# Kernel optimization log

Measured on AMD Instinct MI355X. Metric: run time of the kernel, lower is better.

## Reference

```python
import jax, jax.numpy as jnp
import numpy as np

N = 25000   # nodes
E = 400000  # edges
F_IN = 128  # in_features
F_E = 16    # edge_features
C = 32      # channel_width
F_OUT = 1   # out_features
SLOPE = 0.01  # torch LeakyReLU default negative_slope


def leaky_relu(x):
    return jnp.where(x >= 0, x, SLOPE * x)


def setup_inputs() -> dict:
    key = jax.random.key(0)
    ks = jax.random.split(key, 12)
    x = jax.random.normal(ks[0], (N, F_IN), dtype=jnp.float32)
    edge_index = jax.random.randint(ks[1], (2, E), 0, N, dtype=jnp.int64)
    edge_attr = jax.random.normal(ks[2], (E, F_E), dtype=jnp.float32)
    # parameters (scaled like kaiming-ish fan-in init)
    W_in = jax.random.normal(ks[3], (F_IN, C), dtype=jnp.float32) / np.sqrt(F_IN)
    b_in = jnp.zeros((C,), dtype=jnp.float32)
    W_edge = jax.random.normal(ks[4], (F_E, C * C), dtype=jnp.float32) / np.sqrt(F_E)
    b_edge = jnp.zeros((C * C,), dtype=jnp.float32)
    W_root = jax.random.normal(ks[5], (C, C), dtype=jnp.float32) / np.sqrt(C)
    b_conv = jnp.zeros((C,), dtype=jnp.float32)
    W_out = jax.random.normal(ks[6], (C, F_OUT), dtype=jnp.float32) / np.sqrt(C)
    b_out = jnp.zeros((F_OUT,), dtype=jnp.float32)
    return {
        "x": x, "edge_index": edge_index, "edge_attr": edge_attr,
        "W_in": W_in, "b_in": b_in, "W_edge": W_edge, "b_edge": b_edge,
        "W_root": W_root, "b_conv": b_conv, "W_out": W_out, "b_out": b_out,
    }


def reference(x, edge_index, edge_attr, W_in, b_in, W_edge, b_edge,
              W_root, b_conv, W_out, b_out):
    # input projection (dropout = identity in eval mode)
    h = leaky_relu(x @ W_in + b_in)                       # [N, C]

    # NNConv layer (gnn_depth = 1):
    # per-edge weight matrix from edge_nn: Linear + LeakyReLU
    We = leaky_relu(edge_attr @ W_edge + b_edge)          # [E, C*C]
    We = We.reshape(E, C, C)                              # [E, C, C]
    src, dst = edge_index[0], edge_index[1]               # PyG: j=source, i=target
    # gather source node features, per-edge matvec, scatter-add to targets
    msg = jnp.einsum('ec,eco->eo', h[src], We)            # [E, C]
    aggr = jax.ops.segment_sum(msg, dst, num_segments=N)  # [N, C]
    h = aggr + h @ W_root + b_conv                        # root weight + bias
    h = leaky_relu(h)

    return h @ W_out + b_out                              # [N, F_OUT]
```

## Files before the change

### kernel.cpp

```cpp
#include <hip/hip_runtime.h>

#define NN 25000
#define EE 400000
#define FIN 128
#define FE 16
#define CH 32
#define SLOPE 0.01f

typedef __attribute__((ext_vector_type(8))) short bf16x8;
typedef __attribute__((ext_vector_type(4))) float f32x4;

__device__ __forceinline__ float lrelu(float v) { return fmaxf(v, SLOPE * v); }

__device__ __forceinline__ short f2bf(float f) {
    union { float f; unsigned u; } v; v.f = f;
    unsigned r = (v.u + 0x7fffu + ((v.u >> 16) & 1u)) >> 16;
    return (short)r;
}

__global__ void __launch_bounds__(256)
k_input_proj(const float* __restrict__ x,
             const float* __restrict__ W_in,
             const float* __restrict__ b_in,
             float* __restrict__ h) {
    __shared__ short Wt1[CH * 136];
    int tid = threadIdx.x;
#pragma unroll
    for (int i = 0; i < 16; i++) {
        int id = tid + 256 * i;
        int k = id >> 5, c = id & 31;
        Wt1[c * 136 + k] = f2bf(W_in[id]);
    }
    __syncthreads();

    int wave = tid >> 6, lane = tid & 63;
    int n16 = lane & 15, quad = lane >> 4;
    int node0 = blockIdx.x * 64 + wave * 16;

    f32x4 D[2];
#pragma unroll
    for (int ch = 0; ch < 2; ch++) {
        float bb = b_in[ch * 16 + n16];
        D[ch] = (f32x4){bb, bb, bb, bb};
    }
    int arow = node0 + n16; if (arow >= NN) arow = NN - 1;
#pragma unroll
    for (int kb = 0; kb < 4; kb++) {
        const float4* xp = (const float4*)(x + (size_t)arow * FIN + kb * 32 + quad * 8);
        float4 xa = xp[0], xb = xp[1];
        bf16x8 A = (bf16x8){f2bf(xa.x), f2bf(xa.y), f2bf(xa.z), f2bf(xa.w),
                            f2bf(xb.x), f2bf(xb.y), f2bf(xb.z), f2bf(xb.w)};
#pragma unroll
        for (int ch = 0; ch < 2; ch++) {
            bf16x8 B = *(const bf16x8*)&Wt1[(ch * 16 + n16) * 136 + kb * 32 + quad * 8];
            D[ch] = __builtin_amdgcn_mfma_f32_16x16x32_bf16(A, B, D[ch], 0, 0, 0);
        }
    }
#pragma unroll
    for (int ch = 0; ch < 2; ch++)
#pragma unroll
        for (int r = 0; r < 4; r++) {
            int nn = node0 + quad * 4 + r;
            if (nn < NN) h[(size_t)nn * CH + ch * 16 + n16] = lrelu(D[ch][r]);
        }
}

__global__ void __launch_bounds__(256, 2)
k_edge(const float* __restrict__ ea,
       const float* __restrict__ W_edge,
       const float* __restrict__ b_edge,
       const int* __restrict__ src,
       const int* __restrict__ dst,
       const float* __restrict__ h,
       float* __restrict__ aggr) {
    __shared__ short WtL[1024 * 16];
    __shared__ float bseg[1024];
    __shared__ float hsL[128 * 36];
    __shared__ short zslot[8];

    int tid = threadIdx.x;
    int e0 = blockIdx.x * 128;

    if (tid < 8) zslot[tid] = 0;
#pragma unroll
    for (int i = 0; i < 4; i++) {
        int co = tid + 256 * i;
        short cv[16];
#pragma unroll
        for (int k = 0; k < 16; k++) cv[k] = f2bf(W_edge[k * 1024 + co]);
        ((bf16x8*)&WtL[co * 16])[0] = *(bf16x8*)&cv[0];
        ((bf16x8*)&WtL[co * 16])[1] = *(bf16x8*)&cv[8];
        bseg[co] = b_edge[co];
    }
    {
        int e = tid >> 1, half = tid & 1;
        int s = src[e0 + e];
        const float4* hp = (const float4*)(h + (size_t)s * CH + half * 16);
        float* wdst = &hsL[e * 36 + half * 16];
#pragma unroll
        for (int j = 0; j < 4; j++) *(float4*)(wdst + j * 4) = hp[j];
    }
    __syncthreads();

    int wave = tid >> 6, lane = tid & 63;
    int n16 = lane & 15, quad = lane >> 4;
    int t0 = wave * 32, t1 = wave * 32 + 16;

    bf16x8 A0 = (bf16x8){0,0,0,0,0,0,0,0}, A1 = A0;
    if (quad < 2) {
        const float4* p0 = (const float4*)(ea + (size_t)(e0 + t0 + n16) * FE + quad * 8);
        const float4* p1 = (const float4*)(ea + (size_t)(e0 + t1 + n16) * FE + quad * 8);
        float4 a = p0[0], b = p0[1];
        A0 = (bf16x8){f2bf(a.x), f2bf(a.y), f2bf(a.z), f2bf(a.w),
                      f2bf(b.x), f2bf(b.y), f2bf(b.z), f2bf(b.w)};
        a = p1[0]; b = p1[1];
        A1 = (bf16x8){f2bf(a.x), f2bf(a.y), f2bf(a.z), f2bf(a.w),
                      f2bf(b.x), f2bf(b.y), f2bf(b.z), f2bf(b.w)};
    }

    f32x4 m0[2], m1[2];
    m0[0] = (f32x4){0,0,0,0}; m0[1] = m0[0]; m1[0] = m0[0]; m1[1] = m0[0];

    const short* bbase = (quad < 2) ? WtL : zslot;
    int bstride = (quad < 2) ? 1 : 0;

#pragma unroll 1
    for (int c4 = 0; c4 < 8; c4++) {
        f32x4 hv0[4], hv1[4];
#pragma unroll
        for (int r = 0; r < 4; r++) {
            hv0[r] = *(const f32x4*)&hsL[(t0 + quad * 4 + r) * 36 + c4 * 4];
            hv1[r] = *(const f32x4*)&hsL[(t1 + quad * 4 + r) * 36 + c4 * 4];
        }
#pragma unroll
        for (int cc = 0; cc < 4; cc++) {
            int c = c4 * 4 + cc;
#pragma unroll
            for (int oh = 0; oh < 2; oh++) {
                int cb = c * 2 + oh;
                bf16x8 B = *(const bf16x8*)&bbase[bstride * ((cb * 16 + n16) * 16 + quad * 8)];
                float bb = bseg[cb * 16 + n16];
                f32x4 Cb = (f32x4){bb, bb, bb, bb};
                f32x4 D0 = __builtin_amdgcn_mfma_f32_16x16x32_bf16(A0, B, Cb, 0, 0, 0);
                f32x4 D1 = __builtin_amdgcn_mfma_f32_16x16x32_bf16(A1, B, Cb, 0, 0, 0);
#pragma unroll
                for (int r = 0; r < 4; r++) {
                    m0[oh][r] = fmaf(hv0[r][cc], lrelu(D0[r]), m0[oh][r]);
                    m1[oh][r] = fmaf(hv1[r][cc], lrelu(D1[r]), m1[oh][r]);
                }
            }
        }
    }

#pragma unroll
    for (int r = 0; r < 4; r++) {
        int ed0 = dst[e0 + t0 + quad * 4 + r];
        int ed1 = dst[e0 + t1 + quad * 4 + r];
#pragma unroll
        for (int oh = 0; oh < 2; oh++) {
            unsafeAtomicAdd(&aggr[(size_t)ed0 * CH + oh * 16 + n16], m0[oh][r]);
            unsafeAtomicAdd(&aggr[(size_t)ed1 * CH + oh * 16 + n16], m1[oh][r]);
        }
    }
}

__global__ void k_node(const float* __restrict__ aggr,
                       const float* __restrict__ h,
                       const float* __restrict__ W_root,
                       const float* __restrict__ b_conv,
                       const float* __restrict__ W_out,
                       const float* __restrict__ b_out,
                       float* __restrict__ out) {
    __shared__ float Wr[CH * CH];
    __shared__ float Wo[CH];
    __shared__ float bc[CH];
    int tid = threadIdx.x;
    for (int i = tid; i < CH * CH / 4; i += 256)
        ((float4*)Wr)[i] = ((const float4*)W_root)[i];
    if (tid < CH / 4) ((float4*)Wo)[tid] = ((const float4*)W_out)[tid];
    else if (tid >= 8 && tid < 8 + CH / 4) ((float4*)bc)[tid - 8] = ((const float4*)b_conv)[tid - 8];
    __syncthreads();
    int n = blockIdx.x * 256 + tid;
    if (n >= NN) return;
    float hr[CH], ag[CH];
#pragma unroll
    for (int i = 0; i < CH / 4; i++) {
        ((float4*)hr)[i] = ((const float4*)(h + (size_t)n * CH))[i];
        ((float4*)ag)[i] = ((const float4*)(aggr + (size_t)n * CH))[i];
    }
    float acc = b_out[0];
#pragma unroll 1
    for (int o = 0; o < CH; o++) {
        float t = ag[o] + bc[o];
#pragma unroll
        for (int c = 0; c < CH; c++) t = fmaf(hr[c], Wr[c * CH + o], t);
        acc = fmaf(lrelu(t), Wo[o], acc);
    }
    out[n] = acc;
}

extern "C" void kernel_launch(void* const* d_in, const int* in_sizes, int n_in,
                              void* d_out, int out_size, void* d_ws, size_t ws_size,
                              hipStream_t stream) {
    const float* x      = (const float*)d_in[0];
    const int*   ei     = (const int*)d_in[1];
    const float* ea     = (const float*)d_in[2];
    const float* W_in   = (const float*)d_in[3];
    const float* b_in   = (const float*)d_in[4];
    const float* W_edge = (const float*)d_in[5];
    const float* b_edge = (const float*)d_in[6];
    const float* W_root = (const float*)d_in[7];
    const float* b_conv = (const float*)d_in[8];
    const float* W_out  = (const float*)d_in[9];
    const float* b_out  = (const float*)d_in[10];
    float* out  = (float*)d_out;
    float* h    = (float*)d_ws;
    float* aggr = h + (size_t)NN * CH;

    hipMemsetAsync(aggr, 0, (size_t)NN * CH * sizeof(float), stream);
    k_input_proj<<<(NN + 63) / 64, 256, 0, stream>>>(x, W_in, b_in, h);
    k_edge<<<EE / 128, 256, 0, stream>>>(ea, W_edge, b_edge, ei, ei + EE, h, aggr);
    k_node<<<(NN + 255) / 256, 256, 0, stream>>>(aggr, h, W_root, b_conv, W_out, b_out, out);
}
```

Baseline: 200.8 us.

## Precompute bf16 edge weights and attrs in a fused pre-kernel, raise edge occupancy

The input projection kernel gains auxiliary blocks that transpose W_edge to bf16 once, zero the aggregation buffer in place of a memset, and convert edge_attr to bf16 in global memory. The edge kernel then copies the prepared weight tile with vector loads instead of converting W_edge in every block. It also drops the shared bias array, reading b_edge from global, and raises launch bounds to 3 blocks per CU. The node kernel stores W_root transposed so each output reads contiguous vector rows. The trade-off is an extra bf16 copy of edge_attr written and read back through global memory, plus bias loads moved into the inner loop.

```diff
diff --git a/kernel.cpp b/kernel.cpp
--- a/kernel.cpp
+++ b/kernel.cpp
@@ -6,6 +6,8 @@
 #define FE 16
 #define CH 32
 #define SLOPE 0.01f
+#define PROJ_BLOCKS 391
+#define AUX_BLOCKS 64
 
 typedef __attribute__((ext_vector_type(8))) short bf16x8;
 typedef __attribute__((ext_vector_type(4))) float f32x4;
@@ -19,12 +21,32 @@
 }
 
 __global__ void __launch_bounds__(256)
-k_input_proj(const float* __restrict__ x,
-             const float* __restrict__ W_in,
-             const float* __restrict__ b_in,
-             float* __restrict__ h) {
+k_pre(const float* __restrict__ x, const float* __restrict__ W_in,
+      const float* __restrict__ b_in, const float* __restrict__ ea,
+      const float* __restrict__ W_edge,
+      float* __restrict__ h, float* __restrict__ aggr,
+      short* __restrict__ WtT, short* __restrict__ ea_bf) {
     __shared__ short Wt1[CH * 136];
     int tid = threadIdx.x;
+
+    if (blockIdx.x >= PROJ_BLOCKS) {
+        int t = (blockIdx.x - PROJ_BLOCKS) * 256 + tid;
+        { int co = t >> 4, k = t & 15; WtT[t] = f2bf(W_edge[k * 1024 + co]); }
+        float4 z = make_float4(0.f, 0.f, 0.f, 0.f);
+        for (int i = t; i < NN * CH / 4; i += AUX_BLOCKS * 256) ((float4*)aggr)[i] = z;
+        for (int e = t; e < EE; e += AUX_BLOCKS * 256) {
+            const float4* p = (const float4*)(ea + (size_t)e * FE);
+            float4 a0 = p[0], a1 = p[1], a2 = p[2], a3 = p[3];
+            bf16x8 lo = (bf16x8){f2bf(a0.x), f2bf(a0.y), f2bf(a0.z), f2bf(a0.w),
+                                 f2bf(a1.x), f2bf(a1.y), f2bf(a1.z), f2bf(a1.w)};
+            bf16x8 hi = (bf16x8){f2bf(a2.x), f2bf(a2.y), f2bf(a2.z), f2bf(a2.w),
+                                 f2bf(a3.x), f2bf(a3.y), f2bf(a3.z), f2bf(a3.w)};
+            ((bf16x8*)(ea_bf + (size_t)e * FE))[0] = lo;
+            ((bf16x8*)(ea_bf + (size_t)e * FE))[1] = hi;
+        }
+        return;
+    }
+
 #pragma unroll
     for (int i = 0; i < 16; i++) {
         int id = tid + 256 * i;
@@ -65,16 +87,15 @@
         }
 }
 
-__global__ void __launch_bounds__(256, 2)
-k_edge(const float* __restrict__ ea,
-       const float* __restrict__ W_edge,
+__global__ void __launch_bounds__(256, 3)
+k_edge(const short* __restrict__ WtT,
+       const short* __restrict__ ea_bf,
        const float* __restrict__ b_edge,
        const int* __restrict__ src,
        const int* __restrict__ dst,
        const float* __restrict__ h,
        float* __restrict__ aggr) {
     __shared__ short WtL[1024 * 16];
-    __shared__ float bseg[1024];
     __shared__ float hsL[128 * 36];
     __shared__ short zslot[8];
 
@@ -83,14 +104,9 @@
 
     if (tid < 8) zslot[tid] = 0;
 #pragma unroll
-    for (int i = 0; i < 4; i++) {
-        int co = tid + 256 * i;
-        short cv[16];
-#pragma unroll
-        for (int k = 0; k < 16; k++) cv[k] = f2bf(W_edge[k * 1024 + co]);
-        ((bf16x8*)&WtL[co * 16])[0] = *(bf16x8*)&cv[0];
-        ((bf16x8*)&WtL[co * 16])[1] = *(bf16x8*)&cv[8];
-        bseg[co] = b_edge[co];
+    for (int j = 0; j < 8; j++) {
+        int idx = tid + 256 * j;
+        ((uint4*)WtL)[idx] = ((const uint4*)WtT)[idx];
     }
     {
         int e = tid >> 1, half = tid & 1;
@@ -104,19 +120,11 @@
 
     int wave = tid >> 6, lane = tid & 63;
     int n16 = lane & 15, quad = lane >> 4;
-    int t0 = wave * 32, t1 = wave * 32 + 16;
-
-    bf16x8 A0 = (bf16x8){0,0,0,0,0,0,0,0}, A1 = A0;
-    if (quad < 2) {
-        const float4* p0 = (const float4*)(ea + (size_t)(e0 + t0 + n16) * FE + quad * 8);
-        const float4* p1 = (const float4*)(ea + (size_t)(e0 + t1 + n16) * FE + quad * 8);
-        float4 a = p0[0], b = p0[1];
-        A0 = (bf16x8){f2bf(a.x), f2bf(a.y), f2bf(a.z), f2bf(a.w),
-                      f2bf(b.x), f2bf(b.y), f2bf(b.z), f2bf(b.w)};
-        a = p1[0]; b = p1[1];
-        A1 = (bf16x8){f2bf(a.x), f2bf(a.y), f2bf(a.z), f2bf(a.w),
-                      f2bf(b.x), f2bf(b.y), f2bf(b.z), f2bf(b.w)};
-    }
+    int t0 = wave * 32, t1 = t0 + 16;
+
+    bf16x8 A0 = *(const bf16x8*)(ea_bf + (size_t)(e0 + t0 + n16) * FE + (quad & 1) * 8);
+    bf16x8 A1 = *(const bf16x8*)(ea_bf + (size_t)(e0 + t1 + n16) * FE + (quad & 1) * 8);
+    if (quad >= 2) { A0 = (bf16x8){0,0,0,0,0,0,0,0}; A1 = A0; }
 
     f32x4 m0[2], m1[2];
     m0[0] = (f32x4){0,0,0,0}; m0[1] = m0[0]; m1[0] = m0[0]; m1[1] = m0[0];
@@ -139,7 +147,7 @@
             for (int oh = 0; oh < 2; oh++) {
                 int cb = c * 2 + oh;
                 bf16x8 B = *(const bf16x8*)&bbase[bstride * ((cb * 16 + n16) * 16 + quad * 8)];
-                float bb = bseg[cb * 16 + n16];
+                float bb = b_edge[(cb << 4) + n16];
                 f32x4 Cb = (f32x4){bb, bb, bb, bb};
                 f32x4 D0 = __builtin_amdgcn_mfma_f32_16x16x32_bf16(A0, B, Cb, 0, 0, 0);
                 f32x4 D1 = __builtin_amdgcn_mfma_f32_16x16x32_bf16(A1, B, Cb, 0, 0, 0);
@@ -171,14 +179,16 @@
                        const float* __restrict__ W_out,
                        const float* __restrict__ b_out,
                        float* __restrict__ out) {
-    __shared__ float Wr[CH * CH];
+    __shared__ float WrT[CH * CH];
     __shared__ float Wo[CH];
     __shared__ float bc[CH];
     int tid = threadIdx.x;
-    for (int i = tid; i < CH * CH / 4; i += 256)
-        ((float4*)Wr)[i] = ((const float4*)W_root)[i];
-    if (tid < CH / 4) ((float4*)Wo)[tid] = ((const float4*)W_out)[tid];
-    else if (tid >= 8 && tid < 8 + CH / 4) ((float4*)bc)[tid - 8] = ((const float4*)b_conv)[tid - 8];
+#pragma unroll
+    for (int i = 0; i < 4; i++) {
+        int t = tid + 256 * i;
+        WrT[t] = W_root[(t & 31) * CH + (t >> 5)];
+    }
+    if (tid < CH) { Wo[tid] = W_out[tid]; bc[tid] = b_conv[tid]; }
     __syncthreads();
     int n = blockIdx.x * 256 + tid;
     if (n >= NN) return;
@@ -192,8 +202,14 @@
 #pragma unroll 1
     for (int o = 0; o < CH; o++) {
         float t = ag[o] + bc[o];
-#pragma unroll
-        for (int c = 0; c < CH; c++) t = fmaf(hr[c], Wr[c * CH + o], t);
+        const f32x4* wr = (const f32x4*)&WrT[o * CH];
+#pragma unroll
+        for (int c4 = 0; c4 < 8; c4++) {
+            f32x4 w = wr[c4];
+            const float* hc = &hr[c4 * 4];
+            t = fmaf(hc[0], w[0], t); t = fmaf(hc[1], w[1], t);
+            t = fmaf(hc[2], w[2], t); t = fmaf(hc[3], w[3], t);
+        }
         acc = fmaf(lrelu(t), Wo[o], acc);
     }
     out[n] = acc;
@@ -213,12 +229,14 @@
     const float* b_conv = (const float*)d_in[8];
     const float* W_out  = (const float*)d_in[9];
     const float* b_out  = (const float*)d_in[10];
-    float* out  = (float*)d_out;
-    float* h    = (float*)d_ws;
-    float* aggr = h + (size_t)NN * CH;
-
-    hipMemsetAsync(aggr, 0, (size_t)NN * CH * sizeof(float), stream);
-    k_input_proj<<<(NN + 63) / 64, 256, 0, stream>>>(x, W_in, b_in, h);
-    k_edge<<<EE / 128, 256, 0, stream>>>(ea, W_edge, b_edge, ei, ei + EE, h, aggr);
+    float* out   = (float*)d_out;
+    float* h     = (float*)d_ws;
+    float* aggr  = h + (size_t)NN * CH;
+    short* WtT   = (short*)(aggr + (size_t)NN * CH);
+    short* ea_bf = WtT + 1024 * 16;
+
+    k_pre<<<PROJ_BLOCKS + AUX_BLOCKS, 256, 0, stream>>>(x, W_in, b_in, ea, W_edge,
+                                                        h, aggr, WtT, ea_bf);
+    k_edge<<<EE / 128, 256, 0, stream>>>(WtT, ea_bf, b_edge, ei, ei + EE, h, aggr);
     k_node<<<(NN + 255) / 256, 256, 0, stream>>>(aggr, h, W_root, b_conv, W_out, b_out, out);
 }
```

Measured after the change: 215.1 us. 7.1% more time.

## Precompute packed bf16 edge weights once, fold bias into MFMA, transpose gathered features

Applied to the files above, without the earlier changes.

A new pre-kernel does the input projection and, in extra blocks, converts W_edge plus bias into one packed bf16 table and zeroes the aggregation buffer. This replaces the separate memset and the per-block weight conversion. The edge kernel copies the prepacked table into LDS and folds the bias into the MFMA through a constant-one A element. It stores gathered source features transposed, so each channel is one vector load, and uses a vectorised leaky ReLU. The node kernel transposes W_root for vector LDS reads; the added workspace use and the bf16 rounding of the bias are the trade-offs.

```diff
diff --git a/kernel.cpp b/kernel.cpp
--- a/kernel.cpp
+++ b/kernel.cpp
@@ -6,11 +6,23 @@
 #define FE 16
 #define CH 32
 #define SLOPE 0.01f
+#define PROJ_BLOCKS 391
+#define AUX_BLOCKS 32
+#define WROW 24
+#define WTP_SHORTS (1024 * WROW + 8)
 
 typedef __attribute__((ext_vector_type(8))) short bf16x8;
 typedef __attribute__((ext_vector_type(4))) float f32x4;
 
 __device__ __forceinline__ float lrelu(float v) { return fmaxf(v, SLOPE * v); }
+
+__device__ __forceinline__ f32x4 lrelu4(f32x4 v) {
+    f32x4 s = v * SLOPE;
+    f32x4 r;
+    r[0] = fmaxf(v[0], s[0]); r[1] = fmaxf(v[1], s[1]);
+    r[2] = fmaxf(v[2], s[2]); r[3] = fmaxf(v[3], s[3]);
+    return r;
+}
 
 __device__ __forceinline__ short f2bf(float f) {
     union { float f; unsigned u; } v; v.f = f;
@@ -19,12 +31,35 @@
 }
 
 __global__ void __launch_bounds__(256)
-k_input_proj(const float* __restrict__ x,
-             const float* __restrict__ W_in,
-             const float* __restrict__ b_in,
-             float* __restrict__ h) {
+k_pre(const float* __restrict__ x, const float* __restrict__ W_in,
+      const float* __restrict__ b_in, const float* __restrict__ W_edge,
+      const float* __restrict__ b_edge,
+      float* __restrict__ h, float* __restrict__ aggr, short* __restrict__ WtP) {
     __shared__ short Wt1[CH * 136];
     int tid = threadIdx.x;
+
+    if (blockIdx.x >= PROJ_BLOCKS) {
+        int ab = blockIdx.x - PROJ_BLOCKS;
+        if (ab < 4) {
+            int co = ab * 256 + tid;
+            short row[WROW] __attribute__((aligned(16)));
+#pragma unroll
+            for (int k = 0; k < 16; k++) row[k] = f2bf(W_edge[k * 1024 + co]);
+            row[16] = f2bf(b_edge[co]);
+#pragma unroll
+            for (int k = 17; k < WROW; k++) row[k] = 0;
+            uint4* dstp = (uint4*)(WtP + co * WROW);
+            dstp[0] = ((uint4*)row)[0]; dstp[1] = ((uint4*)row)[1]; dstp[2] = ((uint4*)row)[2];
+            if (ab == 0 && tid < 8) WtP[1024 * WROW + tid] = 0;
+        } else {
+            int t = (ab - 4) * 256 + tid;
+            float4 z = make_float4(0.f, 0.f, 0.f, 0.f);
+            for (int i = t; i < NN * CH / 4; i += (AUX_BLOCKS - 4) * 256)
+                ((float4*)aggr)[i] = z;
+        }
+        return;
+    }
+
 #pragma unroll
     for (int i = 0; i < 16; i++) {
         int id = tid + 256 * i;
@@ -66,88 +101,76 @@
 }
 
 __global__ void __launch_bounds__(256, 2)
-k_edge(const float* __restrict__ ea,
-       const float* __restrict__ W_edge,
-       const float* __restrict__ b_edge,
+k_edge(const short* __restrict__ WtP,
+       const float* __restrict__ ea,
        const int* __restrict__ src,
        const int* __restrict__ dst,
        const float* __restrict__ h,
        float* __restrict__ aggr) {
-    __shared__ short WtL[1024 * 16];
-    __shared__ float bseg[1024];
-    __shared__ float hsL[128 * 36];
-    __shared__ short zslot[8];
+    __shared__ short WtL[WTP_SHORTS];
+    __shared__ float hsT[CH * 132];
 
     int tid = threadIdx.x;
     int e0 = blockIdx.x * 128;
 
-    if (tid < 8) zslot[tid] = 0;
-#pragma unroll
-    for (int i = 0; i < 4; i++) {
-        int co = tid + 256 * i;
-        short cv[16];
-#pragma unroll
-        for (int k = 0; k < 16; k++) cv[k] = f2bf(W_edge[k * 1024 + co]);
-        ((bf16x8*)&WtL[co * 16])[0] = *(bf16x8*)&cv[0];
-        ((bf16x8*)&WtL[co * 16])[1] = *(bf16x8*)&cv[8];
-        bseg[co] = b_edge[co];
+#pragma unroll
+    for (int j = 0; j < 13; j++) {
+        int idx = tid + 256 * j;
+        if (idx < WTP_SHORTS / 8) ((uint4*)WtL)[idx] = ((const uint4*)WtP)[idx];
     }
     {
         int e = tid >> 1, half = tid & 1;
         int s = src[e0 + e];
         const float4* hp = (const float4*)(h + (size_t)s * CH + half * 16);
-        float* wdst = &hsL[e * 36 + half * 16];
-#pragma unroll
-        for (int j = 0; j < 4; j++) *(float4*)(wdst + j * 4) = hp[j];
+        float vv[16] __attribute__((aligned(16)));
+        *(float4*)&vv[0] = hp[0]; *(float4*)&vv[4] = hp[1];
+        *(float4*)&vv[8] = hp[2]; *(float4*)&vv[12] = hp[3];
+#pragma unroll
+        for (int j = 0; j < 16; j++) hsT[(half * 16 + j) * 132 + e] = vv[j];
     }
     __syncthreads();
 
     int wave = tid >> 6, lane = tid & 63;
     int n16 = lane & 15, quad = lane >> 4;
-    int t0 = wave * 32, t1 = wave * 32 + 16;
+    int t0 = wave * 32, t1 = t0 + 16;
 
     bf16x8 A0 = (bf16x8){0,0,0,0,0,0,0,0}, A1 = A0;
     if (quad < 2) {
         const float4* p0 = (const float4*)(ea + (size_t)(e0 + t0 + n16) * FE + quad * 8);
-        const float4* p1 = (const float4*)(ea + (size_t)(e0 + t1 + n16) * FE + quad * 8);
         float4 a = p0[0], b = p0[1];
         A0 = (bf16x8){f2bf(a.x), f2bf(a.y), f2bf(a.z), f2bf(a.w),
                       f2bf(b.x), f2bf(b.y), f2bf(b.z), f2bf(b.w)};
+        const float4* p1 = (const float4*)(ea + (size_t)(e0 + t1 + n16) * FE + quad * 8);
         a = p1[0]; b = p1[1];
         A1 = (bf16x8){f2bf(a.x), f2bf(a.y), f2bf(a.z), f2bf(a.w),
                       f2bf(b.x), f2bf(b.y), f2bf(b.z), f2bf(b.w)};
+    } else if (quad == 2) {
+        A0[0] = (short)0x3F80; A1[0] = (short)0x3F80;
     }
 
     f32x4 m0[2], m1[2];
     m0[0] = (f32x4){0,0,0,0}; m0[1] = m0[0]; m1[0] = m0[0]; m1[1] = m0[0];
-
-    const short* bbase = (quad < 2) ? WtL : zslot;
-    int bstride = (quad < 2) ? 1 : 0;
+    const f32x4 Z = (f32x4){0,0,0,0};
+
+    const short* Bbase = WtL + n16 * WROW + quad * 8;
+    const float* h0b = hsT + t0 + quad * 4;
+    const float* h1b = hsT + t1 + quad * 4;
 
 #pragma unroll 1
     for (int c4 = 0; c4 < 8; c4++) {
-        f32x4 hv0[4], hv1[4];
-#pragma unroll
-        for (int r = 0; r < 4; r++) {
-            hv0[r] = *(const f32x4*)&hsL[(t0 + quad * 4 + r) * 36 + c4 * 4];
-            hv1[r] = *(const f32x4*)&hsL[(t1 + quad * 4 + r) * 36 + c4 * 4];
-        }
 #pragma unroll
         for (int cc = 0; cc < 4; cc++) {
             int c = c4 * 4 + cc;
+            f32x4 hc0 = *(const f32x4*)(h0b + c * 132);
+            f32x4 hc1 = *(const f32x4*)(h1b + c * 132);
 #pragma unroll
             for (int oh = 0; oh < 2; oh++) {
                 int cb = c * 2 + oh;
-                bf16x8 B = *(const bf16x8*)&bbase[bstride * ((cb * 16 + n16) * 16 + quad * 8)];
-                float bb = bseg[cb * 16 + n16];
-                f32x4 Cb = (f32x4){bb, bb, bb, bb};
-                f32x4 D0 = __builtin_amdgcn_mfma_f32_16x16x32_bf16(A0, B, Cb, 0, 0, 0);
-                f32x4 D1 = __builtin_amdgcn_mfma_f32_16x16x32_bf16(A1, B, Cb, 0, 0, 0);
-#pragma unroll
-                for (int r = 0; r < 4; r++) {
-                    m0[oh][r] = fmaf(hv0[r][cc], lrelu(D0[r]), m0[oh][r]);
-                    m1[oh][r] = fmaf(hv1[r][cc], lrelu(D1[r]), m1[oh][r]);
-                }
+                bf16x8 B = *(const bf16x8*)(Bbase + cb * (16 * WROW));
+                f32x4 D0 = __builtin_amdgcn_mfma_f32_16x16x32_bf16(A0, B, Z, 0, 0, 0);
+                f32x4 D1 = __builtin_amdgcn_mfma_f32_16x16x32_bf16(A1, B, Z, 0, 0, 0);
+                m0[oh] += hc0 * lrelu4(D0);
+                m1[oh] += hc1 * lrelu4(D1);
             }
         }
     }
@@ -171,14 +194,16 @@
                        const float* __restrict__ W_out,
                        const float* __restrict__ b_out,
                        float* __restrict__ out) {
-    __shared__ float Wr[CH * CH];
+    __shared__ float WrT[CH * CH];
     __shared__ float Wo[CH];
     __shared__ float bc[CH];
     int tid = threadIdx.x;
-    for (int i = tid; i < CH * CH / 4; i += 256)
-        ((float4*)Wr)[i] = ((const float4*)W_root)[i];
-    if (tid < CH / 4) ((float4*)Wo)[tid] = ((const float4*)W_out)[tid];
-    else if (tid >= 8 && tid < 8 + CH / 4) ((float4*)bc)[tid - 8] = ((const float4*)b_conv)[tid - 8];
+#pragma unroll
+    for (int i = 0; i < 4; i++) {
+        int t = tid + 256 * i;
+        WrT[t] = W_root[(t & 31) * CH + (t >> 5)];
+    }
+    if (tid < CH) { Wo[tid] = W_out[tid]; bc[tid] = b_conv[tid]; }
     __syncthreads();
     int n = blockIdx.x * 256 + tid;
     if (n >= NN) return;
@@ -192,8 +217,14 @@
 #pragma unroll 1
     for (int o = 0; o < CH; o++) {
         float t = ag[o] + bc[o];
-#pragma unroll
-        for (int c = 0; c < CH; c++) t = fmaf(hr[c], Wr[c * CH + o], t);
+        const f32x4* wr = (const f32x4*)&WrT[o * CH];
+#pragma unroll
+        for (int c4 = 0; c4 < 8; c4++) {
+            f32x4 w = wr[c4];
+            const float* hc = &hr[c4 * 4];
+            t = fmaf(hc[0], w[0], t); t = fmaf(hc[1], w[1], t);
+            t = fmaf(hc[2], w[2], t); t = fmaf(hc[3], w[3], t);
+        }
         acc = fmaf(lrelu(t), Wo[o], acc);
     }
     out[n] = acc;
@@ -216,9 +247,10 @@
     float* out  = (float*)d_out;
     float* h    = (float*)d_ws;
     float* aggr = h + (size_t)NN * CH;
-
-    hipMemsetAsync(aggr, 0, (size_t)NN * CH * sizeof(float), stream);
-    k_input_proj<<<(NN + 63) / 64, 256, 0, stream>>>(x, W_in, b_in, h);
-    k_edge<<<EE / 128, 256, 0, stream>>>(ea, W_edge, b_edge, ei, ei + EE, h, aggr);
+    short* WtP  = (short*)(aggr + (size_t)NN * CH);
+
+    k_pre<<<PROJ_BLOCKS + AUX_BLOCKS, 256, 0, stream>>>(x, W_in, b_in, W_edge, b_edge,
+                                                        h, aggr, WtP);
+    k_edge<<<EE / 128, 256, 0, stream>>>(WtP, ea, ei, ei + EE, h, aggr);
     k_node<<<(NN + 255) / 256, 256, 0, stream>>>(aggr, h, W_root, b_conv, W_out, b_out, out);
 }
```

Measured after the change: 189.2 us. 1.06x faster.
